# Performance work log

Measured on AMD Instinct MI355X. Metric: run time of the kernel, lower is better.

The kernel has to match this reference:

```python
import jax, jax.numpy as jnp
import numpy as np

N_USER = 10000
U_DIM = 256
IMG_DIM = 2048
W_DIM = 512
H_DIM = 1024
VOC = 32000
CAP_LEN = 64
SOS = VOC - 2  # <SOS> token id (n_voc_size - 2, as in the torch code)


def setup_inputs() -> dict:
    key = jax.random.key(0)
    ks = jax.random.split(key, 10)
    s = lambda k, shape: jax.random.normal(k, shape, jnp.float32) * 0.02
    return {
        "img_feat": jax.random.normal(ks[0], (1, IMG_DIM), jnp.float32),
        "uid": jax.random.randint(ks[1], (1,), 0, N_USER),
        "wei_user": s(ks[2], (N_USER, U_DIM)),
        "WI_w": s(ks[3], (W_DIM, IMG_DIM + U_DIM)),
        "WI_b": jnp.zeros((W_DIM,), jnp.float32),
        "WP_w": s(ks[4], (VOC, H_DIM)),
        "WP_b": jnp.zeros((VOC,), jnp.float32),
        "W_ih": s(ks[5], (4 * H_DIM, W_DIM)),
        "W_hh": s(ks[6], (4 * H_DIM, H_DIM)),
        "b_ih": jnp.zeros((4 * H_DIM,), jnp.float32),
        "b_hh": jnp.zeros((4 * H_DIM,), jnp.float32),
        "word_emb": s(ks[7], (VOC, W_DIM)),
    }


def _lstm_step(x, h, c, W_ih, W_hh, b_ih, b_hh):
    # torch nn.LSTM gate order: input, forget, cell(g), output
    gates = x @ W_ih.T + b_ih + h @ W_hh.T + b_hh  # [1, 4H]
    i, f, g, o = jnp.split(gates, 4, axis=-1)
    c = jax.nn.sigmoid(f) * c + jax.nn.sigmoid(i) * jnp.tanh(g)
    h = jax.nn.sigmoid(o) * jnp.tanh(c)
    return h, c


def reference(img_feat, uid, wei_user, WI_w, WI_b, WP_w, WP_b,
              W_ih, W_hh, b_ih, b_hh, word_emb):
    # user embedding + image feature -> conditioning input for step 0
    user_emb = wei_user[uid]                                  # [1, U_DIM]
    x0 = jnp.concatenate([img_feat, user_emb], axis=1) @ WI_w.T + WI_b  # [1, W_DIM]

    h = jnp.zeros((1, H_DIM), x0.dtype)
    c = jnp.zeros((1, H_DIM), x0.dtype)
    # prime the LSTM with the image/user conditioning vector
    h, c = _lstm_step(x0, h, c, W_ih, W_hh, b_ih, b_hh)

    def step(carry, _):
        h, c, wid = carry
        x = word_emb[wid]                                     # [1, W_DIM] embedding gather
        h, c = _lstm_step(x, h, c, W_ih, W_hh, b_ih, b_hh)
        logits = h @ WP_w.T + WP_b                            # [1, VOC]
        wid = jnp.argmax(logits, axis=-1).astype(jnp.int32)   # greedy token
        return (h, c, wid), (h, wid[0])

    wid0 = jnp.full((1,), SOS, jnp.int32)
    _, (hiddens, captions) = jax.lax.scan(step, (h, c, wid0), None, length=CAP_LEN)
    # hiddens: [CAP_LEN, 1, H_DIM] (matches torch cat of per-step LSTM outputs)
    return hiddens, captions
```

## Files before the change

kernel.cpp:

```cpp
#include <hip/hip_runtime.h>
#include <hip/hip_bf16.h>
#include <hip/hip_cooperative_groups.h>
#include <math.h>

#define H_DIM 1024
#define W_DIM 512
#define VOC 32000
#define CAP_LEN 64
#define U_DIM 256
#define IMG_DIM 2048
#define XIN_DIM (IMG_DIM + U_DIM)
#define SOS 31998
#define NBLK_LOGITS 512
#define CO_NBLK 512
#define CO_NTHR 512
#define SCOPE_AGENT __HIP_MEMORY_SCOPE_AGENT


__device__ __forceinline__ float wave_reduce_sum(float v) {
    #pragma unroll
    for (int off = 32; off > 0; off >>= 1)
        v += __shfl_xor(v, off, 64);
    return v;
}

__device__ __forceinline__ unsigned long long umax64(unsigned long long a, unsigned long long b) {
    return a > b ? a : b;
}

__device__ __forceinline__ unsigned short f2bf_rne(float f) {
    unsigned u = __float_as_uint(f);
    unsigned rounding = 0x7FFFu + ((u >> 16) & 1u);
    return (unsigned short)((u + rounding) >> 16);
}
__device__ __forceinline__ float bflo(unsigned u) { return __uint_as_float(u << 16); }
__device__ __forceinline__ float bfhi(unsigned u) { return __uint_as_float(u & 0xFFFF0000u); }

__device__ __forceinline__ float ld_coh(const float* p) {
    return __hip_atomic_load(p, __ATOMIC_RELAXED, SCOPE_AGENT);
}
__device__ __forceinline__ void st_coh(float* p, float v) {
    __hip_atomic_store(p, v, __ATOMIC_RELAXED, SCOPE_AGENT);
}
__device__ __forceinline__ unsigned long long ld_coh64(const unsigned long long* p) {
    return __hip_atomic_load(p, __ATOMIC_RELAXED, SCOPE_AGENT);
}
__device__ __forceinline__ void st_coh64(unsigned long long* p, unsigned long long v) {
    __hip_atomic_store(p, v, __ATOMIC_RELAXED, SCOPE_AGENT);
}

__device__ __forceinline__ void gbar(unsigned* leaf, unsigned* root, unsigned* gen,
                                     int bid, unsigned target) {
    __syncthreads();
    if (threadIdx.x == 0) {
        unsigned* lc = leaf + (bid & 7) * 32;
        unsigned old = __hip_atomic_fetch_add(lc, 1u, __ATOMIC_RELAXED, SCOPE_AGENT);
        if (old == (CO_NBLK / 8) - 1) {
            __hip_atomic_store(lc, 0u, __ATOMIC_RELAXED, SCOPE_AGENT);
            unsigned r = __hip_atomic_fetch_add(root, 1u, __ATOMIC_RELAXED, SCOPE_AGENT);
            if (r == 7u) {
                __hip_atomic_store(root, 0u, __ATOMIC_RELAXED, SCOPE_AGENT);
                __hip_atomic_store(gen, target, __ATOMIC_RELEASE, SCOPE_AGENT);
            }
        }
        while (__hip_atomic_load(gen, __ATOMIC_RELAXED, SCOPE_AGENT) < target)
            __builtin_amdgcn_s_sleep(2);
    }
    __syncthreads();
    asm volatile("" ::: "memory");
}

__device__ __forceinline__ float lstm_row_dot(const float* __restrict__ wi,
                                              const float* __restrict__ wh,
                                              const float* __restrict__ x,
                                              const float* __restrict__ h_in,
                                              int lane) {
    float acc = 0.f;
    #pragma unroll
    for (int k = 0; k < 2; ++k) {
        int col = 4 * lane + 256 * k;
        float4 w4 = *reinterpret_cast<const float4*>(wi + col);
        float4 v4 = *reinterpret_cast<const float4*>(x  + col);
        acc += w4.x * v4.x + w4.y * v4.y + w4.z * v4.z + w4.w * v4.w;
    }
    #pragma unroll
    for (int k = 0; k < 4; ++k) {
        int col = 4 * lane + 256 * k;
        float4 w4 = *reinterpret_cast<const float4*>(wh   + col);
        float4 v4 = *reinterpret_cast<const float4*>(h_in + col);
        acc += w4.x * v4.x + w4.y * v4.y + w4.z * v4.z + w4.w * v4.w;
    }
    return wave_reduce_sum(acc);
}

__global__ void k_cvt_wp(const float* __restrict__ src, ushort* __restrict__ dst) {
    int i = blockIdx.x * blockDim.x + threadIdx.x;
    const float4 a = reinterpret_cast<const float4*>(src)[2 * i];
    const float4 b = reinterpret_cast<const float4*>(src)[2 * i + 1];
    union { ushort s[8]; uint4 v; } u;
    u.s[0] = f2bf_rne(a.x); u.s[1] = f2bf_rne(a.y);
    u.s[2] = f2bf_rne(a.z); u.s[3] = f2bf_rne(a.w);
    u.s[4] = f2bf_rne(b.x); u.s[5] = f2bf_rne(b.y);
    u.s[6] = f2bf_rne(b.z); u.s[7] = f2bf_rne(b.w);
    reinterpret_cast<uint4*>(dst)[i] = u.v;
}

__global__ void k_reset(unsigned* bar) {
    bar[threadIdx.x] = 0u;
}

struct CoopParams {
    const float *img, *wei_user, *WI_w, *WI_b, *WP_w, *WP_b,
                *W_ih, *W_hh, *b_ih, *b_hh, *word_emb;
    const int* uid;
    const ushort* WP16;
    unsigned* leaf;
    unsigned* root;
    unsigned* gen;
    float* h_glob;
    float* x0_glob;
    unsigned long long* partial;
    float* out_hid;
    float* out_cap;
    int use_bf16;
};

__global__ void __launch_bounds__(CO_NTHR, 4) k_decode(CoopParams p) {
    const int tid  = threadIdx.x;
    const int bid  = blockIdx.x;
    const int wv   = tid >> 6;
    const int lane = tid & 63;

    __shared__ float lds_xin[XIN_DIM];
    __shared__ float lds_x[W_DIM];
    __shared__ float lds_h[H_DIM];
    __shared__ unsigned long long lds_red[CO_NBLK];
    __shared__ float gsm[2][4];

    unsigned bgen = 0;
    float c_reg = 0.f;

    for (int g = tid; g < XIN_DIM; g += CO_NTHR)
        lds_xin[g] = (g < IMG_DIM) ? p.img[g]
                                   : p.wei_user[(size_t)p.uid[0] * U_DIM + (g - IMG_DIM)];
    __syncthreads();

    {
        int gw = bid * 8 + wv;
        if (gw < 512) {
            const float* wr = p.WI_w + (size_t)gw * XIN_DIM;
            float acc = 0.f;
            #pragma unroll
            for (int k = 0; k < 9; ++k) {
                int col = 4 * lane + 256 * k;
                float4 w4 = *reinterpret_cast<const float4*>(wr + col);
                float4 v4 = *reinterpret_cast<const float4*>(&lds_xin[col]);
                acc += w4.x * v4.x + w4.y * v4.y + w4.z * v4.z + w4.w * v4.w;
            }
            acc = wave_reduce_sum(acc);
            if (lane == 0) st_coh(&p.x0_glob[gw], acc + p.WI_b[gw]);
        }
    }
    gbar(p.leaf, p.root, p.gen, bid, ++bgen);

    if (tid < W_DIM) lds_x[tid] = ld_coh(&p.x0_glob[tid]);
    lds_h[tid] = 0.f;
    __syncthreads();

    auto lstm_phase = [&](const float* x, float* out_hid) {
        const int jslot = wv & 1;
        const int gate  = wv >> 1;
        const int j = bid * 2 + jslot;
        const int row = gate * H_DIM + j;
        float g = lstm_row_dot(p.W_ih + (size_t)row * W_DIM,
                               p.W_hh + (size_t)row * H_DIM, x, lds_h, lane)
                + p.b_ih[row] + p.b_hh[row];
        if (lane == 0) gsm[jslot][gate] = g;
        __syncthreads();
        if (wv < 2 && lane == 0) {
            float gi_ = gsm[wv][0], gf = gsm[wv][1];
            float gg  = gsm[wv][2], go = gsm[wv][3];
            int jj = bid * 2 + wv;
            float ig = 1.f / (1.f + expf(-gi_));
            float fg = 1.f / (1.f + expf(-gf));
            float g_ = tanhf(gg);
            float og = 1.f / (1.f + expf(-go));
            float cn = fg * c_reg + ig * g_;
            float hn = og * tanhf(cn);
            c_reg = cn;
            st_coh(&p.h_glob[jj], hn);
            if (out_hid) out_hid[jj] = hn;
        }
    };

    auto stage_h = [&]() {
        lds_h[tid]       = ld_coh(&p.h_glob[tid]);
        lds_h[tid + 512] = ld_coh(&p.h_glob[tid + 512]);
        __syncthreads();
    };

    auto logits_bf16_phase = [&]() {
        float4 h0a = *reinterpret_cast<const float4*>(&lds_h[8 * lane]);
        float4 h0b = *reinterpret_cast<const float4*>(&lds_h[8 * lane + 4]);
        float4 h1a = *reinterpret_cast<const float4*>(&lds_h[8 * lane + 512]);
        float4 h1b = *reinterpret_cast<const float4*>(&lds_h[8 * lane + 516]);
        const int gw = bid * 8 + wv;
        unsigned long long best = 0ull;
        #pragma unroll
        for (int k = 0; k < 8; ++k) {
            int row = gw + k * 4096;
            if (row < VOC) {
                const uint4* wr = reinterpret_cast<const uint4*>(p.WP16 + (size_t)row * H_DIM);
                uint4 w0 = wr[lane];
                uint4 w1 = wr[lane + 64];
                float acc;
                acc  = bflo(w0.x) * h0a.x + bfhi(w0.x) * h0a.y;
                acc += bflo(w0.y) * h0a.z + bfhi(w0.y) * h0a.w;
                acc += bflo(w0.z) * h0b.x + bfhi(w0.z) * h0b.y;
                acc += bflo(w0.w) * h0b.z + bfhi(w0.w) * h0b.w;
                acc += bflo(w1.x) * h1a.x + bfhi(w1.x) * h1a.y;
                acc += bflo(w1.y) * h1a.z + bfhi(w1.y) * h1a.w;
                acc += bflo(w1.z) * h1b.x + bfhi(w1.z) * h1b.y;
                acc += bflo(w1.w) * h1b.z + bfhi(w1.w) * h1b.w;
                acc = wave_reduce_sum(acc);
                float logit = acc + p.WP_b[row];
                unsigned int ub = __float_as_uint(logit);
                ub = (ub & 0x80000000u) ? ~ub : (ub | 0x80000000u);
                unsigned long long pk = ((unsigned long long)ub << 32)
                                      | (unsigned long long)(0xFFFFFFFFu - (unsigned)row);
                best = umax64(best, pk);
            }
        }
        if (lane == 0) lds_red[wv] = best;
        __syncthreads();
        if (tid == 0) {
            unsigned long long m = lds_red[0];
            #pragma unroll
            for (int i = 1; i < 8; ++i) m = umax64(m, lds_red[i]);
            st_coh64(&p.partial[bid], m);
        }
    };

    auto logits_f32_phase = [&]() {
        const int gw = bid * 8 + wv;
        unsigned long long best = 0ull;
        #pragma unroll
        for (int k = 0; k < 8; ++k) {
            int row = gw + k * 4096;
            if (row < VOC) {
                const float* wr = p.WP_w + (size_t)row * H_DIM;
                float acc = 0.f;
                #pragma unroll
                for (int kk = 0; kk < 4; ++kk) {
                    int col = 4 * lane + 256 * kk;
                    float4 w4 = *reinterpret_cast<const float4*>(wr + col);
                    float4 v4 = *reinterpret_cast<const float4*>(&lds_h[col]);
                    acc += w4.x * v4.x + w4.y * v4.y + w4.z * v4.z + w4.w * v4.w;
                }
                acc = wave_reduce_sum(acc);
                float logit = acc + p.WP_b[row];
                unsigned int ub = __float_as_uint(logit);
                ub = (ub & 0x80000000u) ? ~ub : (ub | 0x80000000u);
                unsigned long long pk = ((unsigned long long)ub << 32)
                                      | (unsigned long long)(0xFFFFFFFFu - (unsigned)row);
                best = umax64(best, pk);
            }
        }
        if (lane == 0) lds_red[wv] = best;
        __syncthreads();
        if (tid == 0) {
            unsigned long long m = lds_red[0];
            #pragma unroll
            for (int i = 1; i < 8; ++i) m = umax64(m, lds_red[i]);
            st_coh64(&p.partial[bid], m);
        }
    };

    auto reduce_wid = [&]() -> int {
        lds_red[tid] = ld_coh64(&p.partial[tid]);
        __syncthreads();
        #pragma unroll
        for (int s = 256; s >= 1; s >>= 1) {
            if (tid < s) lds_red[tid] = umax64(lds_red[tid], lds_red[tid + s]);
            __syncthreads();
        }
        return (int)(0xFFFFFFFFu - (unsigned)(lds_red[0] & 0xFFFFFFFFull));
    };

    lstm_phase(lds_x, nullptr);
    gbar(p.leaf, p.root, p.gen, bid, ++bgen);
    stage_h();

    for (int t = 0; t < CAP_LEN; ++t) {
        if (t > 0) {
            int wid = reduce_wid();
            if (bid == 0 && tid == 0) p.out_cap[t - 1] = (float)wid;
            if (tid < W_DIM) lds_x[tid] = p.word_emb[(size_t)wid * W_DIM + tid];
        } else {
            if (tid < W_DIM) lds_x[tid] = p.word_emb[(size_t)SOS * W_DIM + tid];
        }
        __syncthreads();
        lstm_phase(lds_x, p.out_hid + (size_t)t * H_DIM);
        gbar(p.leaf, p.root, p.gen, bid, ++bgen);
        stage_h();
        if (p.use_bf16) logits_bf16_phase();
        else            logits_f32_phase();
        gbar(p.leaf, p.root, p.gen, bid, ++bgen);
    }
    {
        int wid = reduce_wid();
        if (bid == 0 && tid == 0) p.out_cap[CAP_LEN - 1] = (float)wid;
    }
}

__global__ void k_init(const float* __restrict__ img, const int* __restrict__ uid,
                       const float* __restrict__ wei_user, float* __restrict__ wsf) {
    int i = blockIdx.x * blockDim.x + threadIdx.x;
    if (i < 4096) wsf[i] = 0.f;
    if (i < XIN_DIM) {
        float v = (i < IMG_DIM) ? img[i]
                                : wei_user[(size_t)uid[0] * U_DIM + (i - IMG_DIM)];
        wsf[4096 + i] = v;
    }
}

__global__ void k_x0(const float* __restrict__ WI_w, const float* __restrict__ WI_b,
                     const float* __restrict__ xin, float* __restrict__ x0) {
    int wave = threadIdx.x >> 6;
    int lane = threadIdx.x & 63;
    int row  = blockIdx.x * 4 + wave;
    const float* wr = WI_w + (size_t)row * XIN_DIM;
    float acc = 0.f;
    #pragma unroll
    for (int k = 0; k < 9; ++k) {
        int col = 4 * lane + 256 * k;
        float4 w4 = *reinterpret_cast<const float4*>(wr  + col);
        float4 v4 = *reinterpret_cast<const float4*>(xin + col);
        acc += w4.x * v4.x + w4.y * v4.y + w4.z * v4.z + w4.w * v4.w;
    }
    acc = wave_reduce_sum(acc);
    if (lane == 0) x0[row] = acc + WI_b[row];
}

__global__ void k_lstm(int t,
                       const float* __restrict__ W_ih, const float* __restrict__ W_hh,
                       const float* __restrict__ b_ih, const float* __restrict__ b_hh,
                       const float* __restrict__ word_emb, const float* __restrict__ x0,
                       const unsigned long long* __restrict__ partial,
                       float* __restrict__ out_cap,
                       const float* __restrict__ h_in, const float* __restrict__ c_in,
                       float* __restrict__ h_out, float* __restrict__ c_out,
                       float* __restrict__ out_hid) {
    __shared__ unsigned long long red[256];
    int tid  = threadIdx.x;
    int wave = tid >> 6;
    int lane = tid & 63;
    int j = blockIdx.x * 4 + wave;

    const float* x;
    if (t < 0) {
        x = x0;
    } else if (t == 0) {
        x = word_emb + (size_t)SOS * W_DIM;
    } else {
        red[tid] = umax64(partial[tid], partial[tid + 256]);
        __syncthreads();
        #pragma unroll
        for (int s = 128; s >= 1; s >>= 1) {
            if (tid < s) red[tid] = umax64(red[tid], red[tid + s]);
            __syncthreads();
        }
        int wid = (int)(0xFFFFFFFFu - (unsigned)(red[0] & 0xFFFFFFFFull));
        if (blockIdx.x == 0 && tid == 0) out_cap[t - 1] = (float)wid;
        x = word_emb + (size_t)wid * W_DIM;
    }

    float g[4];
    #pragma unroll
    for (int gi = 0; gi < 4; ++gi) {
        int row = gi * H_DIM + j;
        float acc = lstm_row_dot(W_ih + (size_t)row * W_DIM,
                                 W_hh + (size_t)row * H_DIM, x, h_in, lane);
        g[gi] = acc + b_ih[row] + b_hh[row];
    }
    if (lane == 0) {
        float ig = 1.f / (1.f + expf(-g[0]));
        float fg = 1.f / (1.f + expf(-g[1]));
        float gg = tanhf(g[2]);
        float og = 1.f / (1.f + expf(-g[3]));
        float cn = fg * c_in[j] + ig * gg;
        float hn = og * tanhf(cn);
        c_out[j] = cn;
        h_out[j] = hn;
        if (out_hid) out_hid[j] = hn;
    }
}

__global__ void k_logits_bf16(const ushort* __restrict__ WP16,
                              const float* __restrict__ WP_b,
                              const float* __restrict__ h,
                              unsigned long long* __restrict__ partial) {
    int wave = threadIdx.x >> 6;
    int lane = threadIdx.x & 63;
    int wv = blockIdx.x * 4 + wave;
    float4 h0a = *reinterpret_cast<const float4*>(h + 8 * lane);
    float4 h0b = *reinterpret_cast<const float4*>(h + 8 * lane + 4);
    float4 h1a = *reinterpret_cast<const float4*>(h + 8 * lane + 512);
    float4 h1b = *reinterpret_cast<const float4*>(h + 8 * lane + 516);
    unsigned long long best = 0ull;
    for (int row = wv; row < VOC; row += NBLK_LOGITS * 4) {
        const uint4* wr = reinterpret_cast<const uint4*>(WP16 + (size_t)row * H_DIM);
        uint4 w0 = wr[lane];
        uint4 w1 = wr[lane + 64];
        float acc;
        acc  = bflo(w0.x) * h0a.x + bfhi(w0.x) * h0a.y;
        acc += bflo(w0.y) * h0a.z + bfhi(w0.y) * h0a.w;
        acc += bflo(w0.z) * h0b.x + bfhi(w0.z) * h0b.y;
        acc += bflo(w0.w) * h0b.z + bfhi(w0.w) * h0b.w;
        acc += bflo(w1.x) * h1a.x + bfhi(w1.x) * h1a.y;
        acc += bflo(w1.y) * h1a.z + bfhi(w1.y) * h1a.w;
        acc += bflo(w1.z) * h1b.x + bfhi(w1.z) * h1b.y;
        acc += bflo(w1.w) * h1b.z + bfhi(w1.w) * h1b.w;
        acc = wave_reduce_sum(acc);
        float logit = acc + WP_b[row];
        unsigned int ub = __float_as_uint(logit);
        ub = (ub & 0x80000000u) ? ~ub : (ub | 0x80000000u);
        unsigned long long pk = ((unsigned long long)ub << 32)
                              | (unsigned long long)(0xFFFFFFFFu - (unsigned)row);
        best = umax64(best, pk);
    }
    __shared__ unsigned long long sm[4];
    if (lane == 0) sm[wave] = best;
    __syncthreads();
    if (threadIdx.x == 0)
        partial[blockIdx.x] = umax64(umax64(sm[0], sm[1]), umax64(sm[2], sm[3]));
}

__global__ void k_argmax_final(const unsigned long long* __restrict__ partial,
                               float* __restrict__ out_cap) {
    __shared__ unsigned long long sm[256];
    int tid = threadIdx.x;
    sm[tid] = umax64(partial[tid], partial[tid + 256]);
    __syncthreads();
    for (int s = 128; s > 0; s >>= 1) {
        if (tid < s) sm[tid] = umax64(sm[tid], sm[tid + s]);
        __syncthreads();
    }
    if (tid == 0) {
        int row = (int)(0xFFFFFFFFu - (unsigned)(sm[0] & 0xFFFFFFFFull));
        out_cap[CAP_LEN - 1] = (float)row;
    }
}

extern "C" void kernel_launch(void* const* d_in, const int* in_sizes, int n_in,
                              void* d_out, int out_size, void* d_ws, size_t ws_size,
                              hipStream_t stream) {
    const float* img_feat = (const float*)d_in[0];
    const int*   uid      = (const int*)  d_in[1];
    const float* wei_user = (const float*)d_in[2];
    const float* WI_w     = (const float*)d_in[3];
    const float* WI_b     = (const float*)d_in[4];
    const float* WP_w     = (const float*)d_in[5];
    const float* WP_b     = (const float*)d_in[6];
    const float* W_ih     = (const float*)d_in[7];
    const float* W_hh     = (const float*)d_in[8];
    const float* b_ih     = (const float*)d_in[9];
    const float* b_hh     = (const float*)d_in[10];
    const float* word_emb = (const float*)d_in[11];

    float* out = (float*)d_out;
    float* out_cap = out + CAP_LEN * H_DIM;
    char* ws = (char*)d_ws;

    ushort* WP16 = (ushort*)(ws + (1 << 20));
    const size_t wp16_need = (size_t)(1u << 20) + (size_t)VOC * H_DIM * sizeof(ushort);
    const bool use_bf16 = ws_size >= wp16_need;

    if (use_bf16)
        k_cvt_wp<<<16000, 256, 0, stream>>>(WP_w, WP16);

    k_reset<<<1, 512, 0, stream>>>((unsigned*)ws);

    CoopParams p;
    p.img = img_feat; p.wei_user = wei_user; p.WI_w = WI_w; p.WI_b = WI_b;
    p.WP_w = WP_w; p.WP_b = WP_b; p.W_ih = W_ih; p.W_hh = W_hh;
    p.b_ih = b_ih; p.b_hh = b_hh; p.word_emb = word_emb; p.uid = uid;
    p.WP16 = WP16;
    p.leaf = (unsigned*)ws;
    p.root = (unsigned*)(ws + 1024);
    p.gen  = (unsigned*)(ws + 1152);
    p.h_glob  = (float*)(ws + 2048);
    p.x0_glob = (float*)(ws + 6144);
    p.partial = (unsigned long long*)(ws + 8192);
    p.out_hid = out; p.out_cap = out_cap; p.use_bf16 = use_bf16 ? 1 : 0;

    void* args[] = { &p };
    hipError_t err = hipLaunchCooperativeKernel((const void*)k_decode,
                                                dim3(CO_NBLK), dim3(CO_NTHR),
                                                args, 0, stream);
    if (err != hipSuccess) {
        (void)hipGetLastError();
        float* wsf = (float*)(ws + 16384);
        float* h0 = wsf;
        float* h1 = wsf + 1024;
        float* c0 = wsf + 2048;
        float* c1 = wsf + 3072;
        float* xin = wsf + 4096;
        float* x0  = wsf + 6400;
        unsigned long long* partial = (unsigned long long*)(ws + 16384 + 27904);
        k_init<<<16, 256, 0, stream>>>(img_feat, uid, wei_user, wsf);
        k_x0<<<128, 256, 0, stream>>>(WI_w, WI_b, xin, x0);
        k_lstm<<<256, 256, 0, stream>>>(-1, W_ih, W_hh, b_ih, b_hh, word_emb, x0,
                                        partial, out_cap, h0, c0, h1, c1, nullptr);
        for (int t = 0; t < CAP_LEN; ++t) {
            const float* hi = (t & 1) ? h0 : h1;
            const float* ci = (t & 1) ? c0 : c1;
            float* ho = (t & 1) ? h1 : h0;
            float* co = (t & 1) ? c1 : c0;
            k_lstm<<<256, 256, 0, stream>>>(t, W_ih, W_hh, b_ih, b_hh, word_emb, x0,
                                            partial, out_cap, hi, ci, ho, co,
                                            out + (size_t)t * H_DIM);
            k_logits_bf16<<<NBLK_LOGITS, 256, 0, stream>>>(WP16, WP_b, ho, partial);
        }
        k_argmax_final<<<1, 256, 0, stream>>>(partial, out_cap);
    }
}
```

Before: 1.490 ms.

## Keep LSTM and bf16 projection weights resident in registers across decode steps

```diff
diff --git a/kernel.cpp b/kernel.cpp
--- a/kernel.cpp
+++ b/kernel.cpp
@@ -12,7 +12,7 @@
 #define XIN_DIM (IMG_DIM + U_DIM)
 #define SOS 31998
 #define NBLK_LOGITS 512
-#define CO_NBLK 512
+#define CO_NBLK 256
 #define CO_NTHR 512
 #define SCOPE_AGENT __HIP_MEMORY_SCOPE_AGENT
 
@@ -64,7 +64,7 @@
             }
         }
         while (__hip_atomic_load(gen, __ATOMIC_RELAXED, SCOPE_AGENT) < target)
-            __builtin_amdgcn_s_sleep(2);
+            __builtin_amdgcn_s_sleep(1);
     }
     __syncthreads();
     asm volatile("" ::: "memory");
@@ -110,7 +110,7 @@
 }
 
 struct CoopParams {
-    const float *img, *wei_user, *WI_w, *WI_b, *WP_w, *WP_b,
+    const float *img, *wei_user, *WI_w, *WI_b, *WP_b,
                 *W_ih, *W_hh, *b_ih, *b_hh, *word_emb;
     const int* uid;
     const ushort* WP16;
@@ -122,65 +122,113 @@
     unsigned long long* partial;
     float* out_hid;
     float* out_cap;
-    int use_bf16;
 };
 
-__global__ void __launch_bounds__(CO_NTHR, 4) k_decode(CoopParams p) {
+__global__ void __launch_bounds__(CO_NTHR, 2) k_decode(CoopParams p) {
     const int tid  = threadIdx.x;
     const int bid  = blockIdx.x;
     const int wv   = tid >> 6;
     const int lane = tid & 63;
+    const int gwv  = bid * 8 + wv;
 
     __shared__ float lds_xin[XIN_DIM];
     __shared__ float lds_x[W_DIM];
     __shared__ float lds_h[H_DIM];
-    __shared__ unsigned long long lds_red[CO_NBLK];
-    __shared__ float gsm[2][4];
+    __shared__ unsigned long long lds_red[256];
+    __shared__ float gsm[4][4];
+    __shared__ unsigned long long bsm[8];
 
     unsigned bgen = 0;
     float c_reg = 0.f;
+
+    const int jslot = wv & 3;
+    const int g0 = (wv < 4) ? 0 : 2;
+    const int jj = bid * 4 + jslot;
+    float4 wih[2][2];
+    float4 whh[2][4];
+    float  bih[2], bhh[2];
+    #pragma unroll
+    for (int r = 0; r < 2; ++r) {
+        const int row = (g0 + r) * H_DIM + jj;
+        const float* wi = p.W_ih + (size_t)row * W_DIM;
+        const float* wh = p.W_hh + (size_t)row * H_DIM;
+        wih[r][0] = *reinterpret_cast<const float4*>(wi + 4 * lane);
+        wih[r][1] = *reinterpret_cast<const float4*>(wi + 4 * lane + 256);
+        #pragma unroll
+        for (int k = 0; k < 4; ++k)
+            whh[r][k] = *reinterpret_cast<const float4*>(wh + 4 * lane + 256 * k);
+        bih[r] = p.b_ih[row];
+        bhh[r] = p.b_hh[row];
+    }
+    uint4 wp[16][2];
+    float wpb[16];
+    #pragma unroll
+    for (int k = 0; k < 16; ++k) {
+        const int row = gwv + k * 2048;
+        if (row < VOC) {
+            const uint4* wr = reinterpret_cast<const uint4*>(p.WP16 + (size_t)row * H_DIM);
+            wp[k][0] = wr[lane];
+            wp[k][1] = wr[lane + 64];
+            wpb[k] = p.WP_b[row];
+        } else {
+            uint4 z; z.x = z.y = z.z = z.w = 0u;
+            wp[k][0] = z; wp[k][1] = z; wpb[k] = 0.f;
+        }
+    }
 
     for (int g = tid; g < XIN_DIM; g += CO_NTHR)
         lds_xin[g] = (g < IMG_DIM) ? p.img[g]
                                    : p.wei_user[(size_t)p.uid[0] * U_DIM + (g - IMG_DIM)];
     __syncthreads();
 
-    {
-        int gw = bid * 8 + wv;
-        if (gw < 512) {
-            const float* wr = p.WI_w + (size_t)gw * XIN_DIM;
+    if (wv < 2) {
+        const int gw = bid * 2 + wv;
+        const float* wr = p.WI_w + (size_t)gw * XIN_DIM;
+        float acc = 0.f;
+        #pragma unroll
+        for (int k = 0; k < 9; ++k) {
+            int col = 4 * lane + 256 * k;
+            float4 w4 = *reinterpret_cast<const float4*>(wr + col);
+            float4 v4 = *reinterpret_cast<const float4*>(&lds_xin[col]);
+            acc += w4.x * v4.x + w4.y * v4.y + w4.z * v4.z + w4.w * v4.w;
+        }
+        acc = wave_reduce_sum(acc);
+        if (lane == 0) st_coh(&p.x0_glob[gw], acc + p.WI_b[gw]);
+    }
+    gbar(p.leaf, p.root, p.gen, bid, ++bgen);
+
+    lds_x[tid] = ld_coh(&p.x0_glob[tid] - ((tid < W_DIM) ? 0 : W_DIM));
+    if (tid < W_DIM) lds_x[tid] = ld_coh(&p.x0_glob[tid]);
+    lds_h[tid] = 0.f;
+    lds_h[tid + 512] = 0.f;
+    __syncthreads();
+
+    auto lstm_phase = [&](float* out_hid) {
+        float g[2];
+        #pragma unroll
+        for (int r = 0; r < 2; ++r) {
             float acc = 0.f;
             #pragma unroll
-            for (int k = 0; k < 9; ++k) {
-                int col = 4 * lane + 256 * k;
-                float4 w4 = *reinterpret_cast<const float4*>(wr + col);
-                float4 v4 = *reinterpret_cast<const float4*>(&lds_xin[col]);
+            for (int k = 0; k < 2; ++k) {
+                float4 w4 = wih[r][k];
+                float4 v4 = *reinterpret_cast<const float4*>(&lds_x[4 * lane + 256 * k]);
+                acc += w4.x * v4.x + w4.y * v4.y + w4.z * v4.z + w4.w * v4.w;
+            }
+            #pragma unroll
+            for (int k = 0; k < 4; ++k) {
+                float4 w4 = whh[r][k];
+                float4 v4 = *reinterpret_cast<const float4*>(&lds_h[4 * lane + 256 * k]);
                 acc += w4.x * v4.x + w4.y * v4.y + w4.z * v4.z + w4.w * v4.w;
             }
             acc = wave_reduce_sum(acc);
-            if (lane == 0) st_coh(&p.x0_glob[gw], acc + p.WI_b[gw]);
-        }
-    }
-    gbar(p.leaf, p.root, p.gen, bid, ++bgen);
-
-    if (tid < W_DIM) lds_x[tid] = ld_coh(&p.x0_glob[tid]);
-    lds_h[tid] = 0.f;
-    __syncthreads();
-
-    auto lstm_phase = [&](const float* x, float* out_hid) {
-        const int jslot = wv & 1;
-        const int gate  = wv >> 1;
-        const int j = bid * 2 + jslot;
-        const int row = gate * H_DIM + j;
-        float g = lstm_row_dot(p.W_ih + (size_t)row * W_DIM,
-                               p.W_hh + (size_t)row * H_DIM, x, lds_h, lane)
-                + p.b_ih[row] + p.b_hh[row];
-        if (lane == 0) gsm[jslot][gate] = g;
-        __syncthreads();
-        if (wv < 2 && lane == 0) {
+            g[r] = acc + bih[r] + bhh[r];
+        }
+        if (lane == 0) { gsm[jslot][g0] = g[0]; gsm[jslot][g0 + 1] = g[1]; }
+        __syncthreads();
+        if (wv < 4 && lane == 0) {
             float gi_ = gsm[wv][0], gf = gsm[wv][1];
             float gg  = gsm[wv][2], go = gsm[wv][3];
-            int jj = bid * 2 + wv;
+            int j = bid * 4 + wv;
             float ig = 1.f / (1.f + expf(-gi_));
             float fg = 1.f / (1.f + expf(-gf));
             float g_ = tanhf(gg);
@@ -188,8 +236,8 @@
             float cn = fg * c_reg + ig * g_;
             float hn = og * tanhf(cn);
             c_reg = cn;
-            st_coh(&p.h_glob[jj], hn);
-            if (out_hid) out_hid[jj] = hn;
+            st_coh(&p.h_glob[j], hn);
+            if (out_hid) out_hid[j] = hn;
         }
     };
 
@@ -199,20 +247,18 @@
         __syncthreads();
     };
 
-    auto logits_bf16_phase = [&]() {
+    auto logits_phase = [&]() {
         float4 h0a = *reinterpret_cast<const float4*>(&lds_h[8 * lane]);
         float4 h0b = *reinterpret_cast<const float4*>(&lds_h[8 * lane + 4]);
         float4 h1a = *reinterpret_cast<const float4*>(&lds_h[8 * lane + 512]);
         float4 h1b = *reinterpret_cast<const float4*>(&lds_h[8 * lane + 516]);
-        const int gw = bid * 8 + wv;
         unsigned long long best = 0ull;
         #pragma unroll
-        for (int k = 0; k < 8; ++k) {
-            int row = gw + k * 4096;
+        for (int k = 0; k < 16; ++k) {
+            const int row = gwv + k * 2048;
             if (row < VOC) {
-                const uint4* wr = reinterpret_cast<const uint4*>(p.WP16 + (size_t)row * H_DIM);
-                uint4 w0 = wr[lane];
-                uint4 w1 = wr[lane + 64];
+                uint4 w0 = wp[k][0];
+                uint4 w1 = wp[k][1];
                 float acc;
                 acc  = bflo(w0.x) * h0a.x + bfhi(w0.x) * h0a.y;
                 acc += bflo(w0.y) * h0a.z + bfhi(w0.y) * h0a.w;
@@ -223,7 +269,7 @@
                 acc += bflo(w1.z) * h1b.x + bfhi(w1.z) * h1b.y;
                 acc += bflo(w1.w) * h1b.z + bfhi(w1.w) * h1b.w;
                 acc = wave_reduce_sum(acc);
-                float logit = acc + p.WP_b[row];
+                float logit = acc + wpb[k];
                 unsigned int ub = __float_as_uint(logit);
                 ub = (ub & 0x80000000u) ? ~ub : (ub | 0x80000000u);
                 unsigned long long pk = ((unsigned long long)ub << 32)
@@ -231,63 +277,29 @@
                 best = umax64(best, pk);
             }
         }
-        if (lane == 0) lds_red[wv] = best;
+        if (lane == 0) bsm[wv] = best;
         __syncthreads();
         if (tid == 0) {
-            unsigned long long m = lds_red[0];
+            unsigned long long m = bsm[0];
             #pragma unroll
-            for (int i = 1; i < 8; ++i) m = umax64(m, lds_red[i]);
+            for (int i = 1; i < 8; ++i) m = umax64(m, bsm[i]);
             st_coh64(&p.partial[bid], m);
         }
+        __syncthreads();
     };
 
-    auto logits_f32_phase = [&]() {
-        const int gw = bid * 8 + wv;
-        unsigned long long best = 0ull;
-        #pragma unroll
-        for (int k = 0; k < 8; ++k) {
-            int row = gw + k * 4096;
-            if (row < VOC) {
-                const float* wr = p.WP_w + (size_t)row * H_DIM;
-                float acc = 0.f;
-                #pragma unroll
-                for (int kk = 0; kk < 4; ++kk) {
-                    int col = 4 * lane + 256 * kk;
-                    float4 w4 = *reinterpret_cast<const float4*>(wr + col);
-                    float4 v4 = *reinterpret_cast<const float4*>(&lds_h[col]);
-                    acc += w4.x * v4.x + w4.y * v4.y + w4.z * v4.z + w4.w * v4.w;
-                }
-                acc = wave_reduce_sum(acc);
-                float logit = acc + p.WP_b[row];
-                unsigned int ub = __float_as_uint(logit);
-                ub = (ub & 0x80000000u) ? ~ub : (ub | 0x80000000u);
-                unsigned long long pk = ((unsigned long long)ub << 32)
-                                      | (unsigned long long)(0xFFFFFFFFu - (unsigned)row);
-                best = umax64(best, pk);
-            }
-        }
-        if (lane == 0) lds_red[wv] = best;
-        __syncthreads();
-        if (tid == 0) {
-            unsigned long long m = lds_red[0];
-            #pragma unroll
-            for (int i = 1; i < 8; ++i) m = umax64(m, lds_red[i]);
-            st_coh64(&p.partial[bid], m);
-        }
-    };
-
     auto reduce_wid = [&]() -> int {
-        lds_red[tid] = ld_coh64(&p.partial[tid]);
-        __syncthreads();
-        #pragma unroll
-        for (int s = 256; s >= 1; s >>= 1) {
+        if (tid < 256) lds_red[tid] = ld_coh64(&p.partial[tid]);
+        __syncthreads();
+        #pragma unroll
+        for (int s = 128; s >= 1; s >>= 1) {
             if (tid < s) lds_red[tid] = umax64(lds_red[tid], lds_red[tid + s]);
             __syncthreads();
         }
         return (int)(0xFFFFFFFFu - (unsigned)(lds_red[0] & 0xFFFFFFFFull));
     };
 
-    lstm_phase(lds_x, nullptr);
+    lstm_phase(nullptr);
     gbar(p.leaf, p.root, p.gen, bid, ++bgen);
     stage_h();
 
@@ -300,11 +312,10 @@
             if (tid < W_DIM) lds_x[tid] = p.word_emb[(size_t)SOS * W_DIM + tid];
         }
         __syncthreads();
-        lstm_phase(lds_x, p.out_hid + (size_t)t * H_DIM);
+        lstm_phase(p.out_hid + (size_t)t * H_DIM);
         gbar(p.leaf, p.root, p.gen, bid, ++bgen);
         stage_h();
-        if (p.use_bf16) logits_bf16_phase();
-        else            logits_f32_phase();
+        logits_phase();
         gbar(p.leaf, p.root, p.gen, bid, ++bgen);
     }
     {
@@ -436,6 +447,38 @@
         partial[blockIdx.x] = umax64(umax64(sm[0], sm[1]), umax64(sm[2], sm[3]));
 }
 
+__global__ void k_logits_f32(const float* __restrict__ WP_w, const float* __restrict__ WP_b,
+                             const float* __restrict__ h,
+                             unsigned long long* __restrict__ partial) {
+    int wave = threadIdx.x >> 6;
+    int lane = threadIdx.x & 63;
+    int wv = blockIdx.x * 4 + wave;
+    unsigned long long best = 0ull;
+    for (int row = wv; row < VOC; row += NBLK_LOGITS * 4) {
+        const float* wr = WP_w + (size_t)row * H_DIM;
+        float acc = 0.f;
+        #pragma unroll
+        for (int k = 0; k < 4; ++k) {
+            int col = 4 * lane + 256 * k;
+            float4 w4 = *reinterpret_cast<const float4*>(wr + col);
+            float4 v4 = *reinterpret_cast<const float4*>(h  + col);
+            acc += w4.x * v4.x + w4.y * v4.y + w4.z * v4.z + w4.w * v4.w;
+        }
+        acc = wave_reduce_sum(acc);
+        float logit = acc + WP_b[row];
+        unsigned int ub = __float_as_uint(logit);
+        ub = (ub & 0x80000000u) ? ~ub : (ub | 0x80000000u);
+        unsigned long long pk = ((unsigned long long)ub << 32)
+                              | (unsigned long long)(0xFFFFFFFFu - (unsigned)row);
+        best = umax64(best, pk);
+    }
+    __shared__ unsigned long long sm[4];
+    if (lane == 0) sm[wave] = best;
+    __syncthreads();
+    if (threadIdx.x == 0)
+        partial[blockIdx.x] = umax64(umax64(sm[0], sm[1]), umax64(sm[2], sm[3]));
+}
+
 __global__ void k_argmax_final(const unsigned long long* __restrict__ partial,
                                float* __restrict__ out_cap) {
     __shared__ unsigned long long sm[256];
@@ -476,30 +519,33 @@
     const size_t wp16_need = (size_t)(1u << 20) + (size_t)VOC * H_DIM * sizeof(ushort);
     const bool use_bf16 = ws_size >= wp16_need;
 
-    if (use_bf16)
+    bool coop_ok = false;
+    if (use_bf16) {
         k_cvt_wp<<<16000, 256, 0, stream>>>(WP_w, WP16);
-
-    k_reset<<<1, 512, 0, stream>>>((unsigned*)ws);
-
-    CoopParams p;
-    p.img = img_feat; p.wei_user = wei_user; p.WI_w = WI_w; p.WI_b = WI_b;
-    p.WP_w = WP_w; p.WP_b = WP_b; p.W_ih = W_ih; p.W_hh = W_hh;
-    p.b_ih = b_ih; p.b_hh = b_hh; p.word_emb = word_emb; p.uid = uid;
-    p.WP16 = WP16;
-    p.leaf = (unsigned*)ws;
-    p.root = (unsigned*)(ws + 1024);
-    p.gen  = (unsigned*)(ws + 1152);
-    p.h_glob  = (float*)(ws + 2048);
-    p.x0_glob = (float*)(ws + 6144);
-    p.partial = (unsigned long long*)(ws + 8192);
-    p.out_hid = out; p.out_cap = out_cap; p.use_bf16 = use_bf16 ? 1 : 0;
-
-    void* args[] = { &p };
-    hipError_t err = hipLaunchCooperativeKernel((const void*)k_decode,
-                                                dim3(CO_NBLK), dim3(CO_NTHR),
-                                                args, 0, stream);
-    if (err != hipSuccess) {
-        (void)hipGetLastError();
+        k_reset<<<1, 512, 0, stream>>>((unsigned*)ws);
+
+        CoopParams p;
+        p.img = img_feat; p.wei_user = wei_user; p.WI_w = WI_w; p.WI_b = WI_b;
+        p.WP_b = WP_b; p.W_ih = W_ih; p.W_hh = W_hh;
+        p.b_ih = b_ih; p.b_hh = b_hh; p.word_emb = word_emb; p.uid = uid;
+        p.WP16 = WP16;
+        p.leaf = (unsigned*)ws;
+        p.root = (unsigned*)(ws + 1024);
+        p.gen  = (unsigned*)(ws + 1152);
+        p.h_glob  = (float*)(ws + 2048);
+        p.x0_glob = (float*)(ws + 6144);
+        p.partial = (unsigned long long*)(ws + 8192);
+        p.out_hid = out; p.out_cap = out_cap;
+
+        void* args[] = { &p };
+        hipError_t err = hipLaunchCooperativeKernel((const void*)k_decode,
+                                                    dim3(CO_NBLK), dim3(CO_NTHR),
+                                                    args, 0, stream);
+        coop_ok = (err == hipSuccess);
+        if (!coop_ok) (void)hipGetLastError();
+    }
+
+    if (!coop_ok) {
         float* wsf = (float*)(ws + 16384);
         float* h0 = wsf;
         float* h1 = wsf + 1024;
@@ -520,7 +566,10 @@
             k_lstm<<<256, 256, 0, stream>>>(t, W_ih, W_hh, b_ih, b_hh, word_emb, x0,
                                             partial, out_cap, hi, ci, ho, co,
                                             out + (size_t)t * H_DIM);
-            k_logits_bf16<<<NBLK_LOGITS, 256, 0, stream>>>(WP16, WP_b, ho, partial);
+            if (use_bf16)
+                k_logits_bf16<<<NBLK_LOGITS, 256, 0, stream>>>(WP16, WP_b, ho, partial);
+            else
+                k_logits_f32<<<NBLK_LOGITS, 256, 0, stream>>>(WP_w, WP_b, ho, partial);
         }
         k_argmax_final<<<1, 256, 0, stream>>>(partial, out_cap);
     }
```

Result: slower. 2.185 ms (+46.6%).
